# Performance work log

Hardware: AMD Instinct MI355X
Metric: run time of the kernel (lower is better)

The kernel has to match this reference:

```python
import jax, jax.numpy as jnp
import numpy as np
import math

D_MODEL = 1024
N_DEVICES = 64
HIDDEN = 128
N_HEADS = 8
B, S = 16, 1024
W_SCALE = 0.02

def setup_inputs() -> dict:
    key = jax.random.key(0)
    ks = jax.random.split(key, 24)
    f = jax.random.normal
    inp = {
        'x': f(ks[0], (B, S, D_MODEL), jnp.float32),
        # attention pooling (n_heads=8, non-causal, self-attention) weights, stored [in,out]
        'wq': f(ks[1], (D_MODEL, D_MODEL), jnp.float32) * W_SCALE,
        'bq': jnp.zeros((D_MODEL,), jnp.float32),
        'wk': f(ks[2], (D_MODEL, D_MODEL), jnp.float32) * W_SCALE,
        'bk': jnp.zeros((D_MODEL,), jnp.float32),
        'wv': f(ks[3], (D_MODEL, D_MODEL), jnp.float32) * W_SCALE,
        'bv': jnp.zeros((D_MODEL,), jnp.float32),
        'wo': f(ks[4], (D_MODEL, D_MODEL), jnp.float32) * W_SCALE,
        'bo': jnp.zeros((D_MODEL,), jnp.float32),
        # device embedding table
        'emb': f(ks[5], (N_DEVICES, D_MODEL), jnp.float32),
        # routing gate: Linear(2d,d) -> Tanh -> Linear(d,N) -> Softmax
        'rg_w1': f(ks[6], (2 * D_MODEL, D_MODEL), jnp.float32) * W_SCALE,
        'rg_b1': jnp.zeros((D_MODEL,), jnp.float32),
        'rg_w2': f(ks[7], (D_MODEL, N_DEVICES), jnp.float32) * W_SCALE,
        'rg_b2': jnp.zeros((N_DEVICES,), jnp.float32),
        'reg_w1': f(ks[8], (N_DEVICES, D_MODEL, HIDDEN), jnp.float32) * W_SCALE,
        'reg_b1': jnp.zeros((N_DEVICES, HIDDEN), jnp.float32),
        'reg_w2': f(ks[9], (N_DEVICES, HIDDEN), jnp.float32) * W_SCALE,
        'reg_b2': jnp.zeros((N_DEVICES,), jnp.float32),
        # stacked per-device classification heads: Linear(d,h)->ReLU->Linear(h,1)->Sigmoid
        'cls_w1': f(ks[10], (N_DEVICES, D_MODEL, HIDDEN), jnp.float32) * W_SCALE,
        'cls_b1': jnp.zeros((N_DEVICES, HIDDEN), jnp.float32),
        'cls_w2': f(ks[11], (N_DEVICES, HIDDEN), jnp.float32) * W_SCALE,
        'cls_b2': jnp.zeros((N_DEVICES,), jnp.float32),
    }
    return inp


def _forward(x, wq, bq, wk, bk, wv, bv, wo, bo, emb,
             rg_w1, rg_b1, rg_w2, rg_b2,
             reg_w1, reg_b1, reg_w2, reg_b2,
             cls_w1, cls_b1, cls_w2, cls_b2):
    b, s, d = x.shape
    dk = d // N_HEADS
    scale = 1.0 / math.sqrt(dk)

    def split_heads(t):  # [b,s,d] -> [b,h,s,dk]
        return t.reshape(b, s, N_HEADS, dk).transpose(0, 2, 1, 3)

    Q = split_heads(x @ wq + bq)
    K = split_heads(x @ wk + bk)
    V = split_heads(x @ wv + bv)
    scores = jnp.einsum('bhqd,bhkd->bhqk', Q, K) * scale
    attn = jax.nn.softmax(scores, axis=-1)  # non-causal, no mask, eval (no dropout)
    ctx = jnp.einsum('bhqk,bhkd->bhqd', attn, V)
    ctx = ctx.transpose(0, 2, 1, 3).reshape(b, s, d)
    pooled = ctx @ wo + bo                       # [b,s,d]
    g = pooled.mean(axis=1)                      # [b,d] global_repr

    g_exp = jnp.broadcast_to(g[:, None, :], (b, N_DEVICES, d))
    de_exp = jnp.broadcast_to(emb[None, :, :], (b, N_DEVICES, d))

    # routing gate
    ri = jnp.concatenate([g_exp, de_exp], axis=-1)        # [b,N,2d]
    h = jnp.tanh(ri @ rg_w1 + rg_b1)                      # [b,N,d]
    rw = jax.nn.softmax(h @ rg_w2 + rg_b2, axis=-1)       # [b,N,N]
    device_repr = jnp.einsum('bnm,md->bnd', rw, emb)      # bmm with expanded embeds
    combined = g_exp + device_repr                        # [b,N,d]

    hr = jax.nn.relu(jnp.einsum('bnd,ndh->bnh', combined, reg_w1) + reg_b1)
    reg = jax.nn.softplus(jnp.einsum('bnh,nh->bn', hr, reg_w2) + reg_b2)

    # per-device classification heads (stacked)
    hc = jax.nn.relu(jnp.einsum('bnd,ndh->bnh', combined, cls_w1) + cls_b1)
    cls = jax.nn.sigmoid(jnp.einsum('bnh,nh->bn', hc, cls_w2) + cls_b2)
    return reg, cls


def reference(x, wq, bq, wk, bk, wv, bv, wo, bo, emb,
              rg_w1, rg_b1, rg_w2, rg_b2,
              reg_w1, reg_b1, reg_w2, reg_b2,
              cls_w1, cls_b1, cls_w2, cls_b2):
    return _forward(x, wq, bq, wk, bk, wv, bv, wo, bo, emb,
                    rg_w1, rg_b1, rg_w2, rg_b2,
                    reg_w1, reg_b1, reg_w2, reg_b2,
                    cls_w1, cls_b1, cls_w2, cls_b2)
```

## Files before the change

### kernel.cpp

```cpp
#include <hip/hip_runtime.h>

typedef unsigned short ushort_t;
typedef __attribute__((ext_vector_type(8))) short short8;
typedef __attribute__((ext_vector_type(4))) float floatx4;

__device__ __forceinline__ ushort_t f2bf(float f) {
    unsigned u = __float_as_uint(f);
    return (ushort_t)((u + 0x7fffu + ((u >> 16) & 1u)) >> 16);
}
__device__ __forceinline__ void gll16(const void* g, void* l) {
    __builtin_amdgcn_global_load_lds(
        (const __attribute__((address_space(1))) unsigned int*)g,
        (__attribute__((address_space(3))) unsigned int*)l, 16, 0, 0);
}

__global__ void prep_kernel(const float* __restrict__ x, ushort_t* __restrict__ xb,
                            const float* __restrict__ wq, const float* __restrict__ wk,
                            ushort_t* __restrict__ wqT, ushort_t* __restrict__ wkT) {
    if (blockIdx.y == 0) {
        size_t i = ((size_t)blockIdx.x * 256 + threadIdx.x) * 8;
        float4 v0 = *(const float4*)(x + i);
        float4 v1 = *(const float4*)(x + i + 4);
        uint4 o;
        o.x = (unsigned)f2bf(v0.x) | ((unsigned)f2bf(v0.y) << 16);
        o.y = (unsigned)f2bf(v0.z) | ((unsigned)f2bf(v0.w) << 16);
        o.z = (unsigned)f2bf(v1.x) | ((unsigned)f2bf(v1.y) << 16);
        o.w = (unsigned)f2bf(v1.z) | ((unsigned)f2bf(v1.w) << 16);
        *(uint4*)(xb + i) = o;
    } else {
        int idx = blockIdx.x * 256 + threadIdx.x;
        const float* src = (idx >> 20) ? wk : wq;
        ushort_t* dst = (idx >> 20) ? wkT : wqT;
        int id2 = idx & 1048575;
        int nrow = id2 >> 10, k = id2 & 1023;
        dst[id2] = f2bf(src[k * 1024 + nrow]);
    }
}

__global__ __launch_bounds__(256) void gemm_qk_kernel(
    const ushort_t* __restrict__ xb, const ushort_t* __restrict__ wqT, const ushort_t* __restrict__ wkT,
    const float* __restrict__ bq, const float* __restrict__ bk,
    ushort_t* __restrict__ Qb, ushort_t* __restrict__ Kb)
{
    const int bm = blockIdx.x;
    const int bn = blockIdx.y;
    const int mat = blockIdx.z;
    const ushort_t* W = mat ? wkT : wqT;
    const float* bias = mat ? bk : bq;
    ushort_t* Out = mat ? Kb : Qb;
    const float postscale = mat ? 1.0f : 0.08838834764831845f;

    __shared__ ushort_t a_lds[128 * 32];
    __shared__ ushort_t b_lds[128 * 32];

    const int tid = threadIdx.x;
    const int lane = tid & 63;
    const int wave = tid >> 6;
    const int wr = wave >> 1, wc = wave & 1;
    const int l16 = lane & 15, quad = lane >> 4;

    floatx4 acc[4][4];
    const floatx4 zero4 = {0.f, 0.f, 0.f, 0.f};
#pragma unroll
    for (int i = 0; i < 4; ++i)
#pragma unroll
        for (int j = 0; j < 4; ++j) acc[i][j] = zero4;

    const int srow = wave * 32 + (lane >> 2);
    const int skof = (lane & 3) * 8;
    const ushort_t* gA = xb + (size_t)(bm * 128 + srow) * 1024 + skof;
    const ushort_t* gB = W + (size_t)(bn * 128 + srow) * 1024 + skof;
    ushort_t* lA = &a_lds[wave * 1024];
    ushort_t* lB = &b_lds[wave * 1024];

    for (int kt = 0; kt < 32; ++kt) {
        const int k0 = kt * 32;
        __syncthreads();
        gll16(gA + k0, lA);
        gll16(gA + k0 + 16 * 1024, lA + 512);
        gll16(gB + k0, lB);
        gll16(gB + k0 + 16 * 1024, lB + 512);
        __syncthreads();
        short8 afr[4], bfr[4];
#pragma unroll
        for (int mi = 0; mi < 4; ++mi)
            afr[mi] = *(const short8*)&a_lds[(wr * 64 + mi * 16 + l16) * 32 + quad * 8];
#pragma unroll
        for (int ni = 0; ni < 4; ++ni)
            bfr[ni] = *(const short8*)&b_lds[(wc * 64 + ni * 16 + l16) * 32 + quad * 8];
#pragma unroll
        for (int mi = 0; mi < 4; ++mi)
#pragma unroll
            for (int ni = 0; ni < 4; ++ni)
                acc[mi][ni] = __builtin_amdgcn_mfma_f32_16x16x32_bf16(afr[mi], bfr[ni], acc[mi][ni], 0, 0, 0);
    }
#pragma unroll
    for (int mi = 0; mi < 4; ++mi) {
#pragma unroll
        for (int ni = 0; ni < 4; ++ni) {
            const int gcol = bn * 128 + wc * 64 + ni * 16 + l16;
            const int h = gcol >> 7, d = gcol & 127;
#pragma unroll
            for (int r = 0; r < 4; ++r) {
                const int grow = bm * 128 + wr * 64 + mi * 16 + quad * 4 + r;
                const int b = grow >> 10, s = grow & 1023;
                Out[(((size_t)(b * 8 + h)) * 1024 + s) * 128 + d] =
                    f2bf((acc[mi][ni][r] + bias[gcol]) * postscale);
            }
        }
    }
}

__global__ __launch_bounds__(256) void attn_mfma_kernel(
    const ushort_t* __restrict__ Qb,
    const ushort_t* __restrict__ Kb,
    float* __restrict__ wout)
{
    const int bh = blockIdx.x;
    const int qt = blockIdx.y;
    __shared__ ushort_t ks[2][128 * 128];

    const int tid = threadIdx.x;
    const int wave = tid >> 6, lane = tid & 63;
    const int l16 = lane & 15, quad = lane >> 4;

    const ushort_t* Ksrc = Kb + (size_t)bh * 1024 * 128;

    int srcoff[8];
#pragma unroll
    for (int c = 0; c < 8; ++c) {
        int r = wave * 32 + c * 4 + (lane >> 4);
        int g = (lane & 15) ^ (r & 15);
        srcoff[c] = r * 128 + g * 8;
    }

    auto issue = [&](int buf, int kt) {
        const ushort_t* src = Ksrc + (size_t)kt * 16384;
#pragma unroll
        for (int c = 0; c < 8; ++c)
            gll16(src + srcoff[c], &ks[buf][(wave * 8 + c) * 512]);
    };

    short8 aq[2][4];
    {
        const ushort_t* qsrc = Qb + ((size_t)bh * 1024 + qt * 128 + wave * 32) * 128;
#pragma unroll
        for (int mi = 0; mi < 2; ++mi)
#pragma unroll
            for (int ksp = 0; ksp < 4; ++ksp)
                aq[mi][ksp] = *(const short8*)(qsrc + (size_t)(mi * 16 + l16) * 128 + ksp * 32 + quad * 8);
    }

    const floatx4 zero4 = {0.f, 0.f, 0.f, 0.f};
    float lsum[2][4];
#pragma unroll
    for (int mi = 0; mi < 2; ++mi)
#pragma unroll
        for (int r = 0; r < 4; ++r) lsum[mi][r] = 0.f;

    issue(0, 0);

    for (int kt = 0; kt < 8; ++kt) {
        __syncthreads();
        if (kt < 7) issue((kt + 1) & 1, kt + 1);
        const ushort_t* kbuf = ks[kt & 1];
        floatx4 acc[2][8];
#pragma unroll
        for (int mi = 0; mi < 2; ++mi)
#pragma unroll
            for (int ni = 0; ni < 8; ++ni) acc[mi][ni] = zero4;
#pragma unroll
        for (int ksp = 0; ksp < 4; ++ksp) {
            short8 bk[8];
#pragma unroll
            for (int ni = 0; ni < 8; ++ni) {
                int n = ni * 16 + l16;
                int gs = (ksp * 4 + quad) ^ (n & 15);
                bk[ni] = *(const short8*)&kbuf[n * 128 + gs * 8];
            }
#pragma unroll
            for (int mi = 0; mi < 2; ++mi)
#pragma unroll
                for (int ni = 0; ni < 8; ++ni)
                    acc[mi][ni] = __builtin_amdgcn_mfma_f32_16x16x32_bf16(aq[mi][ksp], bk[ni], acc[mi][ni], 0, 0, 0);
        }
#pragma unroll
        for (int mi = 0; mi < 2; ++mi)
#pragma unroll
            for (int r = 0; r < 4; ++r) {
                float s = 0.f;
#pragma unroll
                for (int ni = 0; ni < 8; ++ni) s += __expf(acc[mi][ni][r]);
                lsum[mi][r] += s;
            }
    }

    issue(0, 0);

    float invl[2][4];
#pragma unroll
    for (int mi = 0; mi < 2; ++mi)
#pragma unroll
        for (int r = 0; r < 4; ++r) {
            float s = lsum[mi][r];
#pragma unroll
            for (int off = 1; off < 16; off <<= 1) s += __shfl_xor(s, off, 16);
            invl[mi][r] = 1.f / s;
        }

    for (int kt = 0; kt < 8; ++kt) {
        __syncthreads();
        if (kt < 7) issue((kt + 1) & 1, kt + 1);
        const ushort_t* kbuf = ks[kt & 1];
        floatx4 acc[2][8];
#pragma unroll
        for (int mi = 0; mi < 2; ++mi)
#pragma unroll
            for (int ni = 0; ni < 8; ++ni) acc[mi][ni] = zero4;
#pragma unroll
        for (int ksp = 0; ksp < 4; ++ksp) {
            short8 bk[8];
#pragma unroll
            for (int ni = 0; ni < 8; ++ni) {
                int n = ni * 16 + l16;
                int gs = (ksp * 4 + quad) ^ (n & 15);
                bk[ni] = *(const short8*)&kbuf[n * 128 + gs * 8];
            }
#pragma unroll
            for (int mi = 0; mi < 2; ++mi)
#pragma unroll
                for (int ni = 0; ni < 8; ++ni)
                    acc[mi][ni] = __builtin_amdgcn_mfma_f32_16x16x32_bf16(aq[mi][ksp], bk[ni], acc[mi][ni], 0, 0, 0);
        }
#pragma unroll
        for (int ni = 0; ni < 8; ++ni) {
            float s = 0.f;
#pragma unroll
            for (int mi = 0; mi < 2; ++mi)
#pragma unroll
                for (int r = 0; r < 4; ++r)
                    s += __expf(acc[mi][ni][r]) * invl[mi][r];
            s += __shfl_xor(s, 16, 64);
            s += __shfl_xor(s, 32, 64);
            if (quad == 0) atomicAdd(&wout[bh * 1024 + kt * 128 + ni * 16 + l16], s);
        }
    }
}

__global__ __launch_bounds__(256) void u_kernel(const float* __restrict__ x,
                                                const float* __restrict__ w,
                                                float* __restrict__ u)
{
    const int b = blockIdx.x, kc = blockIdx.y;
    const int c4 = threadIdx.x;
    const float4* X4 = (const float4*)(x + ((size_t)(b * 1024 + kc * 64)) * 1024);
    float4 acc[8];
#pragma unroll
    for (int h = 0; h < 8; ++h) acc[h] = make_float4(0.f, 0.f, 0.f, 0.f);
    const float* wb = w + b * 8 * 1024 + kc * 64;
    for (int k = 0; k < 64; ++k) {
        float4 xv = X4[(size_t)k * 256 + c4];
#pragma unroll
        for (int h = 0; h < 8; ++h) {
            float ww = wb[h * 1024 + k];
            acc[h].x = fmaf(ww, xv.x, acc[h].x);
            acc[h].y = fmaf(ww, xv.y, acc[h].y);
            acc[h].z = fmaf(ww, xv.z, acc[h].z);
            acc[h].w = fmaf(ww, xv.w, acc[h].w);
        }
    }
#pragma unroll
    for (int h = 0; h < 8; ++h) {
        float* dst = u + ((size_t)(b * 8 + h)) * 1024 + c4 * 4;
        atomicAdd(dst + 0, acc[h].x);
        atomicAdd(dst + 1, acc[h].y);
        atomicAdd(dst + 2, acc[h].z);
        atomicAdd(dst + 3, acc[h].w);
    }
}

__global__ __launch_bounds__(256) void sgemm_kernel(
    const float* __restrict__ A, int lda, long sAz,
    const float* __restrict__ Bm, int ldb, long sBz,
    const float* __restrict__ bias, long sBiasz,
    float* __restrict__ C, int ldc, long sCz,
    int M, int N, int K, float alpha, int nks)
{
    const int z = blockIdx.z;
    const int ks = blockIdx.x % nks;
    const int mt = blockIdx.x / nks;
    const int Kc = K / nks;
    A += (size_t)z * sAz;
    Bm += (size_t)z * sBz;
    C += (size_t)z * sCz;
    const float* bptr = bias ? bias + (size_t)z * sBiasz : nullptr;
    __shared__ float As[64 * 36];
    __shared__ float Bs[32 * 68];
    const int tid = threadIdx.x;
    const int row0 = mt * 64, col0 = blockIdx.y * 64;
    const int ty = tid >> 4, tx = tid & 15;
    float acc[4][4] = {};
    const int aflat = tid * 8;
    const int ar = aflat >> 5, ac = aflat & 31;
    const int br = aflat >> 6, bc = aflat & 63;
    for (int k0 = ks * Kc; k0 < (ks + 1) * Kc; k0 += 32) {
        __syncthreads();
        float4 va0 = make_float4(0.f, 0.f, 0.f, 0.f), va1 = va0;
        if (row0 + ar < M) {
            const float* src = A + (size_t)(row0 + ar) * lda + k0 + ac;
            va0 = *(const float4*)src;
            va1 = *(const float4*)(src + 4);
        }
        *(float4*)&As[ar * 36 + ac] = va0;
        *(float4*)&As[ar * 36 + ac + 4] = va1;
        {
            const float* srcb = Bm + (size_t)(k0 + br) * ldb + col0 + bc;
            *(float4*)&Bs[br * 68 + bc] = *(const float4*)srcb;
            *(float4*)&Bs[br * 68 + bc + 4] = *(const float4*)(srcb + 4);
        }
        __syncthreads();
#pragma unroll
        for (int kk = 0; kk < 32; ++kk) {
            float a0 = As[(ty * 4 + 0) * 36 + kk];
            float a1 = As[(ty * 4 + 1) * 36 + kk];
            float a2 = As[(ty * 4 + 2) * 36 + kk];
            float a3 = As[(ty * 4 + 3) * 36 + kk];
            float b0 = Bs[kk * 68 + tx * 4 + 0];
            float b1 = Bs[kk * 68 + tx * 4 + 1];
            float b2 = Bs[kk * 68 + tx * 4 + 2];
            float b3 = Bs[kk * 68 + tx * 4 + 3];
            acc[0][0] = fmaf(a0, b0, acc[0][0]); acc[0][1] = fmaf(a0, b1, acc[0][1]);
            acc[0][2] = fmaf(a0, b2, acc[0][2]); acc[0][3] = fmaf(a0, b3, acc[0][3]);
            acc[1][0] = fmaf(a1, b0, acc[1][0]); acc[1][1] = fmaf(a1, b1, acc[1][1]);
            acc[1][2] = fmaf(a1, b2, acc[1][2]); acc[1][3] = fmaf(a1, b3, acc[1][3]);
            acc[2][0] = fmaf(a2, b0, acc[2][0]); acc[2][1] = fmaf(a2, b1, acc[2][1]);
            acc[2][2] = fmaf(a2, b2, acc[2][2]); acc[2][3] = fmaf(a2, b3, acc[2][3]);
            acc[3][0] = fmaf(a3, b0, acc[3][0]); acc[3][1] = fmaf(a3, b1, acc[3][1]);
            acc[3][2] = fmaf(a3, b2, acc[3][2]); acc[3][3] = fmaf(a3, b3, acc[3][3]);
        }
    }
#pragma unroll
    for (int i = 0; i < 4; ++i) {
        int r = row0 + ty * 4 + i;
        if (r >= M) continue;
#pragma unroll
        for (int j = 0; j < 4; ++j) {
            int c = col0 + tx * 4 + j;
            float v = alpha * acc[i][j] + ((bptr && ks == 0) ? bptr[c] : 0.f);
            if (nks > 1) atomicAdd(&C[(size_t)r * ldc + c], v);
            else C[(size_t)r * ldc + c] = v;
        }
    }
}

__global__ __launch_bounds__(256) void gate_kernel(
    const float* __restrict__ Ge, const float* __restrict__ Ee, const float* __restrict__ rg_b1,
    const float* __restrict__ rg_w2, const float* __restrict__ rg_b2,
    const float* __restrict__ emb, float* __restrict__ DR)
{
    const int row = blockIdx.x;
    const int b = row >> 6, n = row & 63;
    __shared__ float h[1024];
    __shared__ float red[256];
    __shared__ float rw[64];
    const int tid = threadIdx.x;
    for (int c = tid; c < 1024; c += 256)
        h[c] = tanhf(Ge[b * 1024 + c] + Ee[n * 1024 + c] + rg_b1[c]);
    __syncthreads();
    const int j = tid & 63, ch = tid >> 6;
    float part = 0.f;
    const float* w2p = rg_w2 + (size_t)(ch * 256) * 64 + j;
    for (int c = 0; c < 256; ++c)
        part = fmaf(h[ch * 256 + c], w2p[c * 64], part);
    red[tid] = part;
    __syncthreads();
    if (tid < 64) {
        float lg = red[tid] + red[tid + 64] + red[tid + 128] + red[tid + 192] + rg_b2[j];
        float m = lg;
#pragma unroll
        for (int off = 1; off < 64; off <<= 1) m = fmaxf(m, __shfl_xor(m, off, 64));
        float e = __expf(lg - m);
        float s = e;
#pragma unroll
        for (int off = 1; off < 64; off <<= 1) s += __shfl_xor(s, off, 64);
        rw[tid] = e / s;
    }
    __syncthreads();
    float4 acc = make_float4(0.f, 0.f, 0.f, 0.f);
    const float4* E4 = (const float4*)emb;
    for (int nn = 0; nn < 64; ++nn) {
        float wv = rw[nn];
        float4 ev = E4[nn * 256 + tid];
        acc.x = fmaf(wv, ev.x, acc.x);
        acc.y = fmaf(wv, ev.y, acc.y);
        acc.z = fmaf(wv, ev.z, acc.z);
        acc.w = fmaf(wv, ev.w, acc.w);
    }
    *(float4*)&DR[(size_t)row * 1024 + tid * 4] = acc;
}

__global__ __launch_bounds__(256) void heads_p1_kernel(
    const float* __restrict__ g, const float* __restrict__ DR,
    const float* __restrict__ rw1, const float* __restrict__ cw1,
    float* __restrict__ hpart)
{
    const int n = blockIdx.x, task = blockIdx.y, ksl = blockIdx.z;
    __shared__ float combs[16 * 128];
    const int tid = threadIdx.x;
    for (int i = tid; i < 2048; i += 256) {
        int b = i >> 7, c = i & 127;
        int gc = ksl * 128 + c;
        combs[i] = g[b * 1024 + gc] + DR[((size_t)(b * 64 + n)) * 1024 + gc];
    }
    __syncthreads();
    const int j = tid & 127, sub = tid >> 7;
    const float* W1 = (task ? cw1 : rw1) + (size_t)n * 131072 + (size_t)ksl * 128 * 128;
    float a[8] = {};
    for (int c4 = 0; c4 < 32; ++c4) {
        const float w0 = W1[(c4 * 4 + 0) * 128 + j];
        const float w1 = W1[(c4 * 4 + 1) * 128 + j];
        const float w2 = W1[(c4 * 4 + 2) * 128 + j];
        const float w3 = W1[(c4 * 4 + 3) * 128 + j];
#pragma unroll
        for (int bb = 0; bb < 8; ++bb) {
            float4 cv = *(const float4*)&combs[(sub * 8 + bb) * 128 + c4 * 4];
            a[bb] = fmaf(cv.x, w0, a[bb]);
            a[bb] = fmaf(cv.y, w1, a[bb]);
            a[bb] = fmaf(cv.z, w2, a[bb]);
            a[bb] = fmaf(cv.w, w3, a[bb]);
        }
    }
    float* dst = hpart + (((size_t)(ksl * 2 + task) * 64 + n) * 16 + sub * 8) * 128 + j;
#pragma unroll
    for (int bb = 0; bb < 8; ++bb) dst[bb * 128] = a[bb];
}

__global__ __launch_bounds__(256) void heads_p2_kernel(
    const float* __restrict__ hpart,
    const float* __restrict__ rb1, const float* __restrict__ rw2, const float* __restrict__ rb2,
    const float* __restrict__ cb1, const float* __restrict__ cw2, const float* __restrict__ cb2,
    float* __restrict__ out)
{
    const int n = blockIdx.x, task = blockIdx.y;
    const int tid = threadIdx.x;
    const int b = tid >> 4, jg = tid & 15;
    const float* b1 = (task ? cb1 : rb1) + n * 128 + jg * 8;
    const float* W2 = (task ? cw2 : rw2) + n * 128 + jg * 8;
    float s = 0.f;
#pragma unroll
    for (int k = 0; k < 8; ++k) {
        float h = b1[k];
#pragma unroll
        for (int ksl = 0; ksl < 8; ++ksl)
            h += hpart[(((size_t)(ksl * 2 + task) * 64 + n) * 16 + b) * 128 + jg * 8 + k];
        s = fmaf(fmaxf(h, 0.f), W2[k], s);
    }
#pragma unroll
    for (int off = 1; off < 16; off <<= 1) s += __shfl_xor(s, off, 16);
    if (jg == 0) {
        s += (task ? cb2 : rb2)[n];
        float r = task ? (1.f / (1.f + __expf(-s)))
                       : (fmaxf(s, 0.f) + log1pf(__expf(-fabsf(s))));
        out[task * 1024 + b * 64 + n] = r;
    }
}

extern "C" void kernel_launch(void* const* d_in, const int* in_sizes, int n_in,
                              void* d_out, int out_size, void* d_ws, size_t ws_size,
                              hipStream_t stream)
{
    const float* x      = (const float*)d_in[0];
    const float* wq     = (const float*)d_in[1];
    const float* bq     = (const float*)d_in[2];
    const float* wk     = (const float*)d_in[3];
    const float* bk     = (const float*)d_in[4];
    const float* wv     = (const float*)d_in[5];
    const float* bv     = (const float*)d_in[6];
    const float* wo     = (const float*)d_in[7];
    const float* bo     = (const float*)d_in[8];
    const float* emb    = (const float*)d_in[9];
    const float* rg_w1  = (const float*)d_in[10];
    const float* rg_b1  = (const float*)d_in[11];
    const float* rg_w2  = (const float*)d_in[12];
    const float* rg_b2  = (const float*)d_in[13];
    const float* reg_w1 = (const float*)d_in[14];
    const float* reg_b1 = (const float*)d_in[15];
    const float* reg_w2 = (const float*)d_in[16];
    const float* reg_b2 = (const float*)d_in[17];
    const float* cls_w1 = (const float*)d_in[18];
    const float* cls_b1 = (const float*)d_in[19];
    const float* cls_w2 = (const float*)d_in[20];
    const float* cls_b2 = (const float*)d_in[21];

    char* ws = (char*)d_ws;
    size_t off = 0;
    auto alloc = [&](size_t bytes) { size_t cur = off; off += (bytes + 255) & ~(size_t)255; return cur; };

    ushort_t* xb  = (ushort_t*)(ws + alloc((size_t)16777216 * 2));
    ushort_t* wqT = (ushort_t*)(ws + alloc((size_t)1048576 * 2));
    ushort_t* wkT = (ushort_t*)(ws + alloc((size_t)1048576 * 2));
    ushort_t* Qb  = (ushort_t*)(ws + alloc((size_t)16777216 * 2));
    ushort_t* Kb  = (ushort_t*)(ws + alloc((size_t)16777216 * 2));
    size_t zero_beg = off;
    float* wcol = (float*)(ws + alloc((size_t)131072 * 4));
    float* u    = (float*)(ws + alloc((size_t)131072 * 4));
    float* cm   = (float*)(ws + alloc((size_t)16384 * 4));
    float* gbuf = (float*)(ws + alloc((size_t)16384 * 4));
    float* Ge   = (float*)(ws + alloc((size_t)16384 * 4));
    float* Ee   = (float*)(ws + alloc((size_t)65536 * 4));
    size_t zero_end = off;
    float* DR    = (float*)(ws + alloc((size_t)1048576 * 4));
    float* hpart = (float*)(ws + alloc((size_t)2097152 * 4));

    hipMemsetAsync(ws + zero_beg, 0, zero_end - zero_beg, stream);

    prep_kernel<<<dim3(8192, 2), 256, 0, stream>>>(x, xb, wq, wk, wqT, wkT);
    gemm_qk_kernel<<<dim3(128, 8, 2), 256, 0, stream>>>(xb, wqT, wkT, bq, bk, Qb, Kb);
    attn_mfma_kernel<<<dim3(128, 8), 256, 0, stream>>>(Qb, Kb, wcol);
    u_kernel<<<dim3(16, 16), 256, 0, stream>>>(x, wcol, u);
    sgemm_kernel<<<dim3(4, 2, 8), 256, 0, stream>>>(u, 8192, 1024, wv, 1024, 128, bv, 128,
                                                    cm, 1024, 128, 16, 128, 1024, 1.f / 1024.f, 4);
    sgemm_kernel<<<dim3(8, 16, 1), 256, 0, stream>>>(cm, 1024, 0, wo, 1024, 0, bo, 0,
                                                     gbuf, 1024, 0, 16, 1024, 1024, 1.f, 8);
    sgemm_kernel<<<dim3(8, 16, 1), 256, 0, stream>>>(gbuf, 1024, 0, rg_w1, 1024, 0, nullptr, 0,
                                                     Ge, 1024, 0, 16, 1024, 1024, 1.f, 8);
    sgemm_kernel<<<dim3(8, 16, 1), 256, 0, stream>>>(emb, 1024, 0, rg_w1 + (size_t)1048576, 1024, 0, nullptr, 0,
                                                     Ee, 1024, 0, 64, 1024, 1024, 1.f, 8);
    gate_kernel<<<1024, 256, 0, stream>>>(Ge, Ee, rg_b1, rg_w2, rg_b2, emb, DR);
    heads_p1_kernel<<<dim3(64, 2, 8), 256, 0, stream>>>(gbuf, DR, reg_w1, cls_w1, hpart);
    heads_p2_kernel<<<dim3(64, 2), 256, 0, stream>>>(hpart, reg_b1, reg_w2, reg_b2,
                                                     cls_b1, cls_w2, cls_b2, (float*)d_out);
    (void)in_sizes; (void)n_in; (void)out_size; (void)ws_size;
}
```

Before: 562.4 us.

## Double-buffer QK GEMM, shrink attention K tiles, tiled weight transpose, bf16 x in u_kernel

```diff
diff --git a/kernel.cpp b/kernel.cpp
--- a/kernel.cpp
+++ b/kernel.cpp
@@ -14,26 +14,44 @@
         (__attribute__((address_space(3))) unsigned int*)l, 16, 0, 0);
 }
 
-__global__ void prep_kernel(const float* __restrict__ x, ushort_t* __restrict__ xb,
-                            const float* __restrict__ wq, const float* __restrict__ wk,
-                            ushort_t* __restrict__ wqT, ushort_t* __restrict__ wkT) {
-    if (blockIdx.y == 0) {
-        size_t i = ((size_t)blockIdx.x * 256 + threadIdx.x) * 8;
-        float4 v0 = *(const float4*)(x + i);
-        float4 v1 = *(const float4*)(x + i + 4);
-        uint4 o;
-        o.x = (unsigned)f2bf(v0.x) | ((unsigned)f2bf(v0.y) << 16);
-        o.y = (unsigned)f2bf(v0.z) | ((unsigned)f2bf(v0.w) << 16);
-        o.z = (unsigned)f2bf(v1.x) | ((unsigned)f2bf(v1.y) << 16);
-        o.w = (unsigned)f2bf(v1.z) | ((unsigned)f2bf(v1.w) << 16);
-        *(uint4*)(xb + i) = o;
-    } else {
-        int idx = blockIdx.x * 256 + threadIdx.x;
-        const float* src = (idx >> 20) ? wk : wq;
-        ushort_t* dst = (idx >> 20) ? wkT : wqT;
-        int id2 = idx & 1048575;
-        int nrow = id2 >> 10, k = id2 & 1023;
-        dst[id2] = f2bf(src[k * 1024 + nrow]);
+__global__ void prep_kernel(const float* __restrict__ x, ushort_t* __restrict__ xb) {
+    size_t i = ((size_t)blockIdx.x * 256 + threadIdx.x) * 8;
+    float4 v0 = *(const float4*)(x + i);
+    float4 v1 = *(const float4*)(x + i + 4);
+    uint4 o;
+    o.x = (unsigned)f2bf(v0.x) | ((unsigned)f2bf(v0.y) << 16);
+    o.y = (unsigned)f2bf(v0.z) | ((unsigned)f2bf(v0.w) << 16);
+    o.z = (unsigned)f2bf(v1.x) | ((unsigned)f2bf(v1.y) << 16);
+    o.w = (unsigned)f2bf(v1.z) | ((unsigned)f2bf(v1.w) << 16);
+    *(uint4*)(xb + i) = o;
+}
+
+__global__ __launch_bounds__(256) void transpose_kernel(
+    const float* __restrict__ wq, const float* __restrict__ wk,
+    ushort_t* __restrict__ wqT, ushort_t* __restrict__ wkT)
+{
+    const float* src = blockIdx.z ? wk : wq;
+    ushort_t* dst = blockIdx.z ? wkT : wqT;
+    const int k0 = blockIdx.x * 64, n0 = blockIdx.y * 64;
+    __shared__ float t[64][65];
+    const int tid = threadIdx.x;
+    const int rr = tid >> 4, cc = (tid & 15) * 4;
+#pragma unroll
+    for (int p = 0; p < 4; ++p) {
+        float4 v = *(const float4*)(src + (size_t)(k0 + p * 16 + rr) * 1024 + n0 + cc);
+        t[p * 16 + rr][cc + 0] = v.x;
+        t[p * 16 + rr][cc + 1] = v.y;
+        t[p * 16 + rr][cc + 2] = v.z;
+        t[p * 16 + rr][cc + 3] = v.w;
+    }
+    __syncthreads();
+#pragma unroll
+    for (int p = 0; p < 4; ++p) {
+        int nl = p * 16 + rr;
+        uint2 o;
+        o.x = (unsigned)f2bf(t[cc + 0][nl]) | ((unsigned)f2bf(t[cc + 1][nl]) << 16);
+        o.y = (unsigned)f2bf(t[cc + 2][nl]) | ((unsigned)f2bf(t[cc + 3][nl]) << 16);
+        *(uint2*)(dst + (size_t)(n0 + nl) * 1024 + k0 + cc) = o;
     }
 }
 
@@ -50,8 +68,8 @@
     ushort_t* Out = mat ? Kb : Qb;
     const float postscale = mat ? 1.0f : 0.08838834764831845f;
 
-    __shared__ ushort_t a_lds[128 * 32];
-    __shared__ ushort_t b_lds[128 * 32];
+    __shared__ ushort_t a_lds[2][128 * 32];
+    __shared__ ushort_t b_lds[2][128 * 32];
 
     const int tid = threadIdx.x;
     const int lane = tid & 63;
@@ -70,24 +88,29 @@
     const int skof = (lane & 3) * 8;
     const ushort_t* gA = xb + (size_t)(bm * 128 + srow) * 1024 + skof;
     const ushort_t* gB = W + (size_t)(bn * 128 + srow) * 1024 + skof;
-    ushort_t* lA = &a_lds[wave * 1024];
-    ushort_t* lB = &b_lds[wave * 1024];
-
-    for (int kt = 0; kt < 32; ++kt) {
-        const int k0 = kt * 32;
-        __syncthreads();
+
+    auto issue = [&](int buf, int k0) {
+        ushort_t* lA = &a_lds[buf][wave * 1024];
+        ushort_t* lB = &b_lds[buf][wave * 1024];
         gll16(gA + k0, lA);
         gll16(gA + k0 + 16 * 1024, lA + 512);
         gll16(gB + k0, lB);
         gll16(gB + k0 + 16 * 1024, lB + 512);
+    };
+
+    issue(0, 0);
+    for (int kt = 0; kt < 32; ++kt) {
         __syncthreads();
+        if (kt < 31) issue((kt + 1) & 1, (kt + 1) * 32);
+        const ushort_t* la = a_lds[kt & 1];
+        const ushort_t* lb = b_lds[kt & 1];
         short8 afr[4], bfr[4];
 #pragma unroll
         for (int mi = 0; mi < 4; ++mi)
-            afr[mi] = *(const short8*)&a_lds[(wr * 64 + mi * 16 + l16) * 32 + quad * 8];
+            afr[mi] = *(const short8*)&la[(wr * 64 + mi * 16 + l16) * 32 + quad * 8];
 #pragma unroll
         for (int ni = 0; ni < 4; ++ni)
-            bfr[ni] = *(const short8*)&b_lds[(wc * 64 + ni * 16 + l16) * 32 + quad * 8];
+            bfr[ni] = *(const short8*)&lb[(wc * 64 + ni * 16 + l16) * 32 + quad * 8];
 #pragma unroll
         for (int mi = 0; mi < 4; ++mi)
 #pragma unroll
@@ -111,14 +134,14 @@
     }
 }
 
-__global__ __launch_bounds__(256) void attn_mfma_kernel(
+__global__ __launch_bounds__(256, 4) void attn_mfma_kernel(
     const ushort_t* __restrict__ Qb,
     const ushort_t* __restrict__ Kb,
     float* __restrict__ wout)
 {
     const int bh = blockIdx.x;
     const int qt = blockIdx.y;
-    __shared__ ushort_t ks[2][128 * 128];
+    __shared__ ushort_t ks[2][64 * 128];
 
     const int tid = threadIdx.x;
     const int wave = tid >> 6, lane = tid & 63;
@@ -126,19 +149,19 @@
 
     const ushort_t* Ksrc = Kb + (size_t)bh * 1024 * 128;
 
-    int srcoff[8];
-#pragma unroll
-    for (int c = 0; c < 8; ++c) {
-        int r = wave * 32 + c * 4 + (lane >> 4);
+    int srcoff[4];
+#pragma unroll
+    for (int c = 0; c < 4; ++c) {
+        int r = wave * 16 + c * 4 + (lane >> 4);
         int g = (lane & 15) ^ (r & 15);
         srcoff[c] = r * 128 + g * 8;
     }
 
     auto issue = [&](int buf, int kt) {
-        const ushort_t* src = Ksrc + (size_t)kt * 16384;
-#pragma unroll
-        for (int c = 0; c < 8; ++c)
-            gll16(src + srcoff[c], &ks[buf][(wave * 8 + c) * 512]);
+        const ushort_t* src = Ksrc + (size_t)kt * 8192;
+#pragma unroll
+        for (int c = 0; c < 4; ++c)
+            gll16(src + srcoff[c], &ks[buf][(wave * 4 + c) * 512]);
     };
 
     short8 aq[2][4];
@@ -160,20 +183,20 @@
 
     issue(0, 0);
 
-    for (int kt = 0; kt < 8; ++kt) {
+    for (int kt = 0; kt < 16; ++kt) {
         __syncthreads();
-        if (kt < 7) issue((kt + 1) & 1, kt + 1);
+        if (kt < 15) issue((kt + 1) & 1, kt + 1);
         const ushort_t* kbuf = ks[kt & 1];
-        floatx4 acc[2][8];
+        floatx4 acc[2][4];
 #pragma unroll
         for (int mi = 0; mi < 2; ++mi)
 #pragma unroll
-            for (int ni = 0; ni < 8; ++ni) acc[mi][ni] = zero4;
+            for (int ni = 0; ni < 4; ++ni) acc[mi][ni] = zero4;
 #pragma unroll
         for (int ksp = 0; ksp < 4; ++ksp) {
-            short8 bk[8];
-#pragma unroll
-            for (int ni = 0; ni < 8; ++ni) {
+            short8 bk[4];
+#pragma unroll
+            for (int ni = 0; ni < 4; ++ni) {
                 int n = ni * 16 + l16;
                 int gs = (ksp * 4 + quad) ^ (n & 15);
                 bk[ni] = *(const short8*)&kbuf[n * 128 + gs * 8];
@@ -181,7 +204,7 @@
 #pragma unroll
             for (int mi = 0; mi < 2; ++mi)
 #pragma unroll
-                for (int ni = 0; ni < 8; ++ni)
+                for (int ni = 0; ni < 4; ++ni)
                     acc[mi][ni] = __builtin_amdgcn_mfma_f32_16x16x32_bf16(aq[mi][ksp], bk[ni], acc[mi][ni], 0, 0, 0);
         }
 #pragma unroll
@@ -190,7 +213,7 @@
             for (int r = 0; r < 4; ++r) {
                 float s = 0.f;
 #pragma unroll
-                for (int ni = 0; ni < 8; ++ni) s += __expf(acc[mi][ni][r]);
+                for (int ni = 0; ni < 4; ++ni) s += __expf(acc[mi][ni][r]);
                 lsum[mi][r] += s;
             }
     }
@@ -208,20 +231,20 @@
             invl[mi][r] = 1.f / s;
         }
 
-    for (int kt = 0; kt < 8; ++kt) {
+    for (int kt = 0; kt < 16; ++kt) {
         __syncthreads();
-        if (kt < 7) issue((kt + 1) & 1, kt + 1);
+        if (kt < 15) issue((kt + 1) & 1, kt + 1);
         const ushort_t* kbuf = ks[kt & 1];
-        floatx4 acc[2][8];
+        floatx4 acc[2][4];
 #pragma unroll
         for (int mi = 0; mi < 2; ++mi)
 #pragma unroll
-            for (int ni = 0; ni < 8; ++ni) acc[mi][ni] = zero4;
+            for (int ni = 0; ni < 4; ++ni) acc[mi][ni] = zero4;
 #pragma unroll
         for (int ksp = 0; ksp < 4; ++ksp) {
-            short8 bk[8];
-#pragma unroll
-            for (int ni = 0; ni < 8; ++ni) {
+            short8 bk[4];
+#pragma unroll
+            for (int ni = 0; ni < 4; ++ni) {
                 int n = ni * 16 + l16;
                 int gs = (ksp * 4 + quad) ^ (n & 15);
                 bk[ni] = *(const short8*)&kbuf[n * 128 + gs * 8];
@@ -229,11 +252,11 @@
 #pragma unroll
             for (int mi = 0; mi < 2; ++mi)
 #pragma unroll
-                for (int ni = 0; ni < 8; ++ni)
+                for (int ni = 0; ni < 4; ++ni)
                     acc[mi][ni] = __builtin_amdgcn_mfma_f32_16x16x32_bf16(aq[mi][ksp], bk[ni], acc[mi][ni], 0, 0, 0);
         }
 #pragma unroll
-        for (int ni = 0; ni < 8; ++ni) {
+        for (int ni = 0; ni < 4; ++ni) {
             float s = 0.f;
 #pragma unroll
             for (int mi = 0; mi < 2; ++mi)
@@ -242,31 +265,35 @@
                     s += __expf(acc[mi][ni][r]) * invl[mi][r];
             s += __shfl_xor(s, 16, 64);
             s += __shfl_xor(s, 32, 64);
-            if (quad == 0) atomicAdd(&wout[bh * 1024 + kt * 128 + ni * 16 + l16], s);
-        }
-    }
-}
-
-__global__ __launch_bounds__(256) void u_kernel(const float* __restrict__ x,
+            if (quad == 0) atomicAdd(&wout[bh * 1024 + kt * 64 + ni * 16 + l16], s);
+        }
+    }
+}
+
+__global__ __launch_bounds__(256) void u_kernel(const ushort_t* __restrict__ xb,
                                                 const float* __restrict__ w,
                                                 float* __restrict__ u)
 {
     const int b = blockIdx.x, kc = blockIdx.y;
     const int c4 = threadIdx.x;
-    const float4* X4 = (const float4*)(x + ((size_t)(b * 1024 + kc * 64)) * 1024);
+    const ushort_t* Xp = xb + ((size_t)(b * 1024 + kc * 64)) * 1024 + c4 * 4;
     float4 acc[8];
 #pragma unroll
     for (int h = 0; h < 8; ++h) acc[h] = make_float4(0.f, 0.f, 0.f, 0.f);
     const float* wb = w + b * 8 * 1024 + kc * 64;
     for (int k = 0; k < 64; ++k) {
-        float4 xv = X4[(size_t)k * 256 + c4];
+        uint2 uv = *(const uint2*)(Xp + (size_t)k * 1024);
+        float x0 = __uint_as_float(uv.x << 16);
+        float x1 = __uint_as_float(uv.x & 0xffff0000u);
+        float x2 = __uint_as_float(uv.y << 16);
+        float x3 = __uint_as_float(uv.y & 0xffff0000u);
 #pragma unroll
         for (int h = 0; h < 8; ++h) {
             float ww = wb[h * 1024 + k];
-            acc[h].x = fmaf(ww, xv.x, acc[h].x);
-            acc[h].y = fmaf(ww, xv.y, acc[h].y);
-            acc[h].z = fmaf(ww, xv.z, acc[h].z);
-            acc[h].w = fmaf(ww, xv.w, acc[h].w);
+            acc[h].x = fmaf(ww, x0, acc[h].x);
+            acc[h].y = fmaf(ww, x1, acc[h].y);
+            acc[h].z = fmaf(ww, x2, acc[h].z);
+            acc[h].w = fmaf(ww, x3, acc[h].w);
         }
     }
 #pragma unroll
@@ -514,10 +541,11 @@
 
     hipMemsetAsync(ws + zero_beg, 0, zero_end - zero_beg, stream);
 
-    prep_kernel<<<dim3(8192, 2), 256, 0, stream>>>(x, xb, wq, wk, wqT, wkT);
+    prep_kernel<<<8192, 256, 0, stream>>>(x, xb);
+    transpose_kernel<<<dim3(16, 16, 2), 256, 0, stream>>>(wq, wk, wqT, wkT);
     gemm_qk_kernel<<<dim3(128, 8, 2), 256, 0, stream>>>(xb, wqT, wkT, bq, bk, Qb, Kb);
     attn_mfma_kernel<<<dim3(128, 8), 256, 0, stream>>>(Qb, Kb, wcol);
-    u_kernel<<<dim3(16, 16), 256, 0, stream>>>(x, wcol, u);
+    u_kernel<<<dim3(16, 16), 256, 0, stream>>>(xb, wcol, u);
     sgemm_kernel<<<dim3(4, 2, 8), 256, 0, stream>>>(u, 8192, 1024, wv, 1024, 128, bv, 128,
                                                     cm, 1024, 128, 16, 128, 1024, 1.f / 1024.f, 4);
     sgemm_kernel<<<dim3(8, 16, 1), 256, 0, stream>>>(cm, 1024, 0, wo, 1024, 0, bo, 0,
```

Result: faster. 523.4 us (-6.9%).
